# Optimization experiments

Measured on AMD Instinct MI355X. Metric: run time of the kernel, lower is better.

The kernel has to match this reference:

```python
import jax, jax.numpy as jnp
import numpy as np

B, C, H, W = 64, 8, 256, 256
EMB, LAT = 64, 32


def affine_grid(theta, Hh, Ww):
    # F.affine_grid, align_corners=False. theta: [N,2,3] -> grid [N,H,W,2] (x,y)
    xs = (jnp.arange(Ww, dtype=theta.dtype) + 0.5) * (2.0 / Ww) - 1.0
    ys = (jnp.arange(Hh, dtype=theta.dtype) + 0.5) * (2.0 / Hh) - 1.0
    X, Y = jnp.meshgrid(xs, ys)  # [H,W]
    base = jnp.stack([X, Y, jnp.ones_like(X)], axis=-1)  # [H,W,3]
    return jnp.einsum('hwk,nik->nhwi', base, theta)


def grid_sample(img, grid):
    # F.grid_sample bilinear, padding_mode='zeros', align_corners=False
    # img: [N,C,H,W], grid: [N,H,W,2]
    N, Cc, Hh, Ww = img.shape
    ix = ((grid[..., 0] + 1.0) * Ww - 1.0) * 0.5
    iy = ((grid[..., 1] + 1.0) * Hh - 1.0) * 0.5
    x0 = jnp.floor(ix)
    y0 = jnp.floor(iy)
    wx1 = ix - x0
    wy1 = iy - y0
    wx0 = 1.0 - wx1
    wy0 = 1.0 - wy1

    def gather(xf, yf):
        xi = xf.astype(jnp.int32)
        yi = yf.astype(jnp.int32)
        valid = ((xi >= 0) & (xi < Ww) & (yi >= 0) & (yi < Hh)).astype(img.dtype)
        xc = jnp.clip(xi, 0, Ww - 1)
        yc = jnp.clip(yi, 0, Hh - 1)

        def one(im, yb, xb, vb):
            return im[:, yb, xb] * vb[None]  # [C,H,W]

        return jax.vmap(one)(img, yc, xc, valid)

    v00 = gather(x0, y0)
    v01 = gather(x0 + 1.0, y0)
    v10 = gather(x0, y0 + 1.0)
    v11 = gather(x0 + 1.0, y0 + 1.0)
    w00 = (wy0 * wx0)[:, None]
    w01 = (wy0 * wx1)[:, None]
    w10 = (wy1 * wx0)[:, None]
    w11 = (wy1 * wx1)[:, None]
    return v00 * w00 + v01 * w01 + v10 * w10 + v11 * w11


def setup_inputs() -> dict:
    key = jax.random.key(0)
    ks = jax.random.split(key, 9)
    return {
        'x': jax.random.normal(ks[0], (B, C, H, W), jnp.float32),
        'W_ae': jax.random.normal(ks[1], (C, EMB), jnp.float32) * 0.1,
        'W_rot': jax.random.normal(ks[2], (EMB, 6), jnp.float32) * 0.1,
        'W_scale': jax.random.normal(ks[3], (EMB, 6), jnp.float32) * 0.1,
        'W_shear': jax.random.normal(ks[4], (EMB, 6), jnp.float32) * 0.1,
        'W_trans': jax.random.normal(ks[5], (EMB, 6), jnp.float32) * 0.1,
        'W_mask': jax.random.normal(ks[6], (EMB, 1), jnp.float32) * 0.1,
        'W_enc': jax.random.normal(ks[7], (C, LAT), jnp.float32) * 0.1,
        'W_dec': jax.random.normal(ks[8], (C, C), jnp.float32) * 0.1,
    }


def reference(x, W_ae, W_rot, W_scale, W_shear, W_trans, W_mask, W_enc, W_dec):
    Bb, Cc, Hh, Ww = x.shape
    # affine_encoder: global-average-pool + linear
    emb_affine = x.mean(axis=(2, 3)) @ W_ae  # [B,EMB]
    eye = jnp.array([[1.0, 0.0, 0.0], [0.0, 1.0, 0.0]], x.dtype)
    head = lambda Wt: (emb_affine @ Wt).reshape(Bb, 2, 3) * 0.1 + eye
    rotation = head(W_rot)
    scale = head(W_scale)
    shear = head(W_shear)
    translation = head(W_trans)
    mask_parameter = jax.nn.sigmoid(emb_affine @ W_mask)[:, :, None, None]  # [B,1,1,1]

    # affine_transform: four sequential affine_grid + grid_sample passes, then mask
    xt = x
    for theta in (rotation, scale, shear, translation):
        grid = affine_grid(theta, Hh, Ww)
        xt = grid_sample(xt, grid)
    xt = xt * mask_parameter

    emb = xt.mean(axis=(2, 3)) @ W_enc  # encoder on transformed image
    x_dec = jnp.einsum('bchw,cd->bdhw', xt, W_dec)  # pointwise-linear decoder
    return (x_dec, emb, scale, shear, rotation, translation, mask_parameter)
```

## Files before the change

### kernel.cpp

```cpp
#include <hip/hip_runtime.h>
#include <hip/hip_fp16.h>
#include <math.h>

#define BB   64
#define CC   8
#define HH   256
#define WW   256
#define EMB  64
#define LAT  32
#define HW   (HH*WW)
#define PLANE 65536
#define IMG  (CC*HW)

#define OFF_XDEC  0
#define OFF_EMB   33554432
#define OFF_SCALE 33556480
#define OFF_SHEAR 33556864
#define OFF_ROT   33557248
#define OFF_TRANS 33557632
#define OFF_MASK  33558016

#define WS_SUMS   0
#define WS_THETA  512
#define WS_MASK   2048
#define WS_ACC    2112
#define WS_BUF0   4096
#define WS_BUF1   (4096 + 16777216)

#define TH 16
#define TW 64
#define SR 20
#define SC 68
#define SN (SR*SC)

__global__ void k_zero(float* __restrict__ ws) {
    ws[WS_SUMS + threadIdx.x] = 0.f;
}

__device__ __forceinline__ unsigned pack2(float a, float b) {
    __half2 t = __floats2half2_rn(a, b);
    return *(unsigned*)&t;
}
__device__ __forceinline__ float2 up2(unsigned v) {
    __half2 h = *(__half2*)&v;
    return __half22float2(h);
}

__global__ void k_meanT(const float* __restrict__ x, uint4* __restrict__ outp,
                        float* __restrict__ sums) {
    int bid = blockIdx.x;
    int b = bid >> 6;
    int hq = bid & 63;
    int r = threadIdx.x >> 6;
    int lane = threadIdx.x & 63;
    int h = hq * 4 + r;
    const float* ib = x + (size_t)b * IMG + h * WW + 4 * lane;
    float4 v0 = *(const float4*)(ib + 0 * PLANE);
    float4 v1 = *(const float4*)(ib + 1 * PLANE);
    float4 v2 = *(const float4*)(ib + 2 * PLANE);
    float4 v3 = *(const float4*)(ib + 3 * PLANE);
    float4 v4 = *(const float4*)(ib + 4 * PLANE);
    float4 v5 = *(const float4*)(ib + 5 * PLANE);
    float4 v6 = *(const float4*)(ib + 6 * PLANE);
    float4 v7 = *(const float4*)(ib + 7 * PLANE);

    uint4* ob = outp + (size_t)b * HW + h * WW + 4 * lane;
#define PIXOUT(J, COMP) { uint4 u; \
    u.x = pack2(v0.COMP, v1.COMP); u.y = pack2(v2.COMP, v3.COMP); \
    u.z = pack2(v4.COMP, v5.COMP); u.w = pack2(v6.COMP, v7.COMP); ob[J] = u; }
    PIXOUT(0, x) PIXOUT(1, y) PIXOUT(2, z) PIXOUT(3, w)
#undef PIXOUT

    float p[CC];
    p[0] = (v0.x + v0.y) + (v0.z + v0.w);
    p[1] = (v1.x + v1.y) + (v1.z + v1.w);
    p[2] = (v2.x + v2.y) + (v2.z + v2.w);
    p[3] = (v3.x + v3.y) + (v3.z + v3.w);
    p[4] = (v4.x + v4.y) + (v4.z + v4.w);
    p[5] = (v5.x + v5.y) + (v5.z + v5.w);
    p[6] = (v6.x + v6.y) + (v6.z + v6.w);
    p[7] = (v7.x + v7.y) + (v7.z + v7.w);

    __shared__ float part[4][CC];
    #pragma unroll
    for (int ch = 0; ch < CC; ch++) {
        float v = p[ch];
        for (int off = 32; off > 0; off >>= 1) v += __shfl_down(v, off, 64);
        if (lane == 0) part[r][ch] = v;
    }
    __syncthreads();
    if (threadIdx.x < CC) {
        float v = (part[0][threadIdx.x] + part[1][threadIdx.x]) +
                  (part[2][threadIdx.x] + part[3][threadIdx.x]);
        atomicAdd(&sums[b * CC + threadIdx.x], v);
    }
}

__global__ void k_params(const float* __restrict__ sums,
                         const float* __restrict__ W_ae, const float* __restrict__ W_rot,
                         const float* __restrict__ W_scale, const float* __restrict__ W_shear,
                         const float* __restrict__ W_trans, const float* __restrict__ W_mask,
                         float* __restrict__ ws, float* __restrict__ out) {
    int b = blockIdx.x;
    int t = threadIdx.x;

    if (t < CC) ws[WS_ACC + b * CC + t] = 0.f;

    __shared__ float emb_s[EMB];
    {
        float s = 0.f;
        #pragma unroll
        for (int c = 0; c < CC; c++)
            s += (sums[b * CC + c] * (1.0f / (float)HW)) * W_ae[c * EMB + t];
        emb_s[t] = s;
    }
    __syncthreads();

    if (t < 24) {
        int h = t / 6, k = t % 6;
        const float* Wt = (h == 0) ? W_rot : (h == 1) ? W_scale : (h == 2) ? W_shear : W_trans;
        float s = 0.f;
        #pragma unroll
        for (int e = 0; e < EMB; e++) s += emb_s[e] * Wt[e * 6 + k];
        const float eyev = (k == 0 || k == 4) ? 1.0f : 0.0f;
        float th = s * 0.1f + eyev;
        ws[WS_THETA + h * (BB * 6) + b * 6 + k] = th;
        int off = (h == 0) ? OFF_ROT : (h == 1) ? OFF_SCALE : (h == 2) ? OFF_SHEAR : OFF_TRANS;
        out[off + b * 6 + k] = th;
    } else if (t == 24) {
        float s = 0.f;
        #pragma unroll
        for (int e = 0; e < EMB; e++) s += emb_s[e] * W_mask[e];
        float mk = 1.0f / (1.0f + expf(-s));
        ws[WS_MASK + b] = mk;
        out[OFF_MASK + b] = mk;
    }
}

struct Corners {
    int x0c, x1c, y0c, y1c;
    float w00, w01, w10, w11;
};

__device__ __forceinline__ Corners affine_corners(float t00, float t01, float t02,
                                                  float t10, float t11, float t12,
                                                  int gh, int gw) {
    float X = ((float)gw + 0.5f) * (2.0f / (float)WW) - 1.0f;
    float Y = ((float)gh + 0.5f) * (2.0f / (float)HH) - 1.0f;
    float gx = X * t00 + Y * t01 + t02;
    float gy = X * t10 + Y * t11 + t12;
    float ix = ((gx + 1.0f) * (float)WW - 1.0f) * 0.5f;
    float iy = ((gy + 1.0f) * (float)HH - 1.0f) * 0.5f;
    float x0f = floorf(ix), y0f = floorf(iy);
    int x0 = (int)x0f, y0 = (int)y0f, x1 = x0 + 1, y1 = y0 + 1;
    float wx1 = ix - x0f, wy1 = iy - y0f, wx0 = 1.f - wx1, wy0 = 1.f - wy1;
    float fx0 = ((unsigned)x0 < (unsigned)WW) ? 1.f : 0.f;
    float fx1 = ((unsigned)x1 < (unsigned)WW) ? 1.f : 0.f;
    float fy0 = ((unsigned)y0 < (unsigned)HH) ? 1.f : 0.f;
    float fy1 = ((unsigned)y1 < (unsigned)HH) ? 1.f : 0.f;
    Corners c;
    c.x0c = min(max(x0, 0), WW - 1); c.x1c = min(max(x1, 0), WW - 1);
    c.y0c = min(max(y0, 0), HH - 1); c.y1c = min(max(y1, 0), HH - 1);
    c.w00 = wy0*wx0*fy0*fx0; c.w01 = wy0*wx1*fy0*fx1;
    c.w10 = wy1*wx0*fy1*fx0; c.w11 = wy1*wx1*fy1*fx1;
    return c;
}

__device__ __forceinline__ uint4 bilerp8_pk(uint4 a00, uint4 a01, uint4 a10, uint4 a11,
                                            __half2 h00, __half2 h01, __half2 h10, __half2 h11) {
    uint4 u;
#define BLEND(COMP) { \
    __half2 r = __hmul2(*(__half2*)&a00.COMP, h00); \
    r = __hfma2(*(__half2*)&a01.COMP, h01, r); \
    r = __hfma2(*(__half2*)&a10.COMP, h10, r); \
    r = __hfma2(*(__half2*)&a11.COMP, h11, r); \
    u.COMP = *(unsigned*)&r; }
    BLEND(x) BLEND(y) BLEND(z) BLEND(w)
#undef BLEND
    return u;
}

__device__ __forceinline__ int lidx(int sr, int sc) {
    sr = min(max(sr, 0), SR - 1);
    sc = min(max(sc, 0), SC - 1);
    return sr * SC + (sc ^ ((sc >> 3) & 7));
}

__device__ __forceinline__ void stage_g2l(uint4* __restrict__ buf,
                                          const uint4* __restrict__ pb,
                                          const float* __restrict__ th,
                                          int oh, int ow, int tid) {
    float t00 = th[0], t01 = th[1], t02 = th[2], t10 = th[3], t11 = th[4], t12 = th[5];
    for (int i = tid; i < SN; i += 256) {
        int lr = i / SC, lc = i - lr * SC;
        Corners c = affine_corners(t00, t01, t02, t10, t11, t12, oh - 2 + lr, ow - 2 + lc);
        uint4 a00 = pb[c.y0c * WW + c.x0c], a01 = pb[c.y0c * WW + c.x1c];
        uint4 a10 = pb[c.y1c * WW + c.x0c], a11 = pb[c.y1c * WW + c.x1c];
        __half2 h00 = __float2half2_rn(c.w00), h01 = __float2half2_rn(c.w01);
        __half2 h10 = __float2half2_rn(c.w10), h11 = __float2half2_rn(c.w11);
        buf[lr * SC + (lc ^ ((lc >> 3) & 7))] =
            bilerp8_pk(a00, a01, a10, a11, h00, h01, h10, h11);
    }
}

__global__ __launch_bounds__(256) void k_warpA(const uint4* __restrict__ in,
                                               uint4* __restrict__ out,
                                               const float* __restrict__ ws) {
    __shared__ uint4 buf[SN];
    int bid = blockIdx.x;
    int b = bid >> 6;
    int tile = bid & 63;
    int oh = (tile >> 2) * TH;
    int ow = (tile & 3) * TW;
    int tid = threadIdx.x;
    const uint4* pb = in + (size_t)b * HW;

    stage_g2l(buf, pb, ws + WS_THETA + 0 * (BB * 6) + b * 6, oh, ow, tid);
    __syncthreads();

    const float* th = ws + WS_THETA + 1 * (BB * 6) + b * 6;
    float t00 = th[0], t01 = th[1], t02 = th[2], t10 = th[3], t11 = th[4], t12 = th[5];
    uint4* ob = out + (size_t)b * HW;
    for (int i = tid; i < TH * TW; i += 256) {
        int lr = i >> 6, lc = i & 63;
        int gh = oh + lr, gw = ow + lc;
        Corners c = affine_corners(t00, t01, t02, t10, t11, t12, gh, gw);
        uint4 a00 = buf[lidx(c.y0c - oh + 2, c.x0c - ow + 2)];
        uint4 a01 = buf[lidx(c.y0c - oh + 2, c.x1c - ow + 2)];
        uint4 a10 = buf[lidx(c.y1c - oh + 2, c.x0c - ow + 2)];
        uint4 a11 = buf[lidx(c.y1c - oh + 2, c.x1c - ow + 2)];
        __half2 h00 = __float2half2_rn(c.w00), h01 = __float2half2_rn(c.w01);
        __half2 h10 = __float2half2_rn(c.w10), h11 = __float2half2_rn(c.w11);
        ob[gh * WW + gw] = bilerp8_pk(a00, a01, a10, a11, h00, h01, h10, h11);
    }
}

__global__ __launch_bounds__(256) void k_warpB(const uint4* __restrict__ in,
                                               const float* __restrict__ ws,
                                               const float* __restrict__ W_dec,
                                               float* __restrict__ out,
                                               float* __restrict__ acc) {
    __shared__ uint4 buf[SN];
    __shared__ float Wd[CC * CC];
    __shared__ float part[4][CC];
    int bid = blockIdx.x;
    int b = bid >> 6;
    int tile = bid & 63;
    int oh = (tile >> 2) * TH;
    int ow = (tile & 3) * TW;
    int tid = threadIdx.x;
    if (tid < CC * CC) Wd[tid] = W_dec[tid];
    const uint4* pb = in + (size_t)b * HW;

    stage_g2l(buf, pb, ws + WS_THETA + 2 * (BB * 6) + b * 6, oh, ow, tid);
    __syncthreads();

    float mk = ws[WS_MASK + b];
    const float* th = ws + WS_THETA + 3 * (BB * 6) + b * 6;
    float t00 = th[0], t01 = th[1], t02 = th[2], t10 = th[3], t11 = th[4], t12 = th[5];

    int wv = tid >> 6, lane = tid & 63;
    int r = wv * 4 + (lane >> 4);
    int c0 = (lane & 15) * 4;
    float sl[CC];
    #pragma unroll
    for (int ch = 0; ch < CC; ch++) sl[ch] = 0.f;
    float od[CC][4];

    #pragma unroll
    for (int px = 0; px < 4; px++) {
        int gh = oh + r, gw = ow + c0 + px;
        Corners c = affine_corners(t00, t01, t02, t10, t11, t12, gh, gw);
        uint4 a00 = buf[lidx(c.y0c - oh + 2, c.x0c - ow + 2)];
        uint4 a01 = buf[lidx(c.y0c - oh + 2, c.x1c - ow + 2)];
        uint4 a10 = buf[lidx(c.y1c - oh + 2, c.x0c - ow + 2)];
        uint4 a11 = buf[lidx(c.y1c - oh + 2, c.x1c - ow + 2)];
        __half2 h00 = __float2half2_rn(c.w00 * mk), h01 = __float2half2_rn(c.w01 * mk);
        __half2 h10 = __float2half2_rn(c.w10 * mk), h11 = __float2half2_rn(c.w11 * mk);
        uint4 u = bilerp8_pk(a00, a01, a10, a11, h00, h01, h10, h11);

        float2 s01 = up2(u.x), s23 = up2(u.y), s45 = up2(u.z), s67 = up2(u.w);
        float s[CC] = {s01.x, s01.y, s23.x, s23.y, s45.x, s45.y, s67.x, s67.y};

        #pragma unroll
        for (int ch = 0; ch < CC; ch++) sl[ch] += s[ch];
        #pragma unroll
        for (int d = 0; d < CC; d++) {
            float rr = 0.f;
            #pragma unroll
            for (int ch = 0; ch < CC; ch++) rr += s[ch] * Wd[ch * CC + d];
            od[d][px] = rr;
        }
    }

    size_t base = (size_t)b * IMG + (size_t)(oh + r) * WW + (ow + c0);
    #pragma unroll
    for (int d = 0; d < CC; d++) {
        float4 f4 = make_float4(od[d][0], od[d][1], od[d][2], od[d][3]);
        *(float4*)(out + OFF_XDEC + base + d * PLANE) = f4;
    }

    #pragma unroll
    for (int ch = 0; ch < CC; ch++) {
        float v = sl[ch];
        for (int off = 32; off > 0; off >>= 1) v += __shfl_down(v, off, 64);
        if (lane == 0) part[wv][ch] = v;
    }
    __syncthreads();
    if (tid < CC) {
        float v = (part[0][tid] + part[1][tid]) + (part[2][tid] + part[3][tid]);
        atomicAdd(&acc[b * CC + tid], v);
    }
}

__global__ void k_emb(const float* __restrict__ acc, const float* __restrict__ W_enc,
                      float* __restrict__ out) {
    for (int i = threadIdx.x; i < BB * LAT; i += 256) {
        int b = i >> 5, l = i & 31;
        float s = 0.f;
        #pragma unroll
        for (int c = 0; c < CC; c++)
            s += (acc[b * CC + c] * (1.0f / (float)HW)) * W_enc[c * LAT + l];
        out[OFF_EMB + i] = s;
    }
}

extern "C" void kernel_launch(void* const* d_in, const int* in_sizes, int n_in,
                              void* d_out, int out_size, void* d_ws, size_t ws_size,
                              hipStream_t stream) {
    const float* x       = (const float*)d_in[0];
    const float* W_ae    = (const float*)d_in[1];
    const float* W_rot   = (const float*)d_in[2];
    const float* W_scale = (const float*)d_in[3];
    const float* W_shear = (const float*)d_in[4];
    const float* W_trans = (const float*)d_in[5];
    const float* W_mask  = (const float*)d_in[6];
    const float* W_enc   = (const float*)d_in[7];
    const float* W_dec   = (const float*)d_in[8];

    float* ws   = (float*)d_ws;
    float* out  = (float*)d_out;
    float* sums = ws + WS_SUMS;
    float* acc  = ws + WS_ACC;
    uint4* hb0  = (uint4*)(ws + WS_BUF0);
    uint4* hb1  = (uint4*)(ws + WS_BUF1);

    k_zero<<<1, 512, 0, stream>>>(ws);
    k_meanT<<<BB * (HH / 4), 256, 0, stream>>>(x, hb0, sums);
    k_params<<<BB, 64, 0, stream>>>(sums, W_ae, W_rot, W_scale, W_shear, W_trans, W_mask, ws, out);
    k_warpA<<<BB * 64, 256, 0, stream>>>(hb0, hb1, ws);
    k_warpB<<<BB * 64, 256, 0, stream>>>(hb1, ws, W_dec, out, acc);
    k_emb<<<1, 256, 0, stream>>>(acc, W_enc, out);
}
```

Before: 150.3 us.

## Double warp tile height to 32 rows with 512-thread blocks and packed-FMA decoder

Raises the output tile in both warp kernels from 16 to 32 rows and the block size to 512 threads, so the 2-row staging halo is a smaller share of each tile and less redundant first-pass resampling is done. In the second warp kernel the 8x8 decoder matmul now uses two-wide float vector FMAs with weights stored as pairs in shared memory, which may map to packed FMA instructions. Larger LDS per block (about 39KB) and half as many blocks may lower occupancy and leave fewer blocks per CU for load balancing.

```diff
diff --git a/kernel.cpp b/kernel.cpp
--- a/kernel.cpp
+++ b/kernel.cpp
@@ -27,11 +27,13 @@
 #define WS_BUF0   4096
 #define WS_BUF1   (4096 + 16777216)
 
-#define TH 16
+#define TH 32
 #define TW 64
-#define SR 20
+#define SR 36
 #define SC 68
 #define SN (SR*SC)
+
+typedef float v2f __attribute__((ext_vector_type(2)));
 
 __global__ void k_zero(float* __restrict__ ws) {
     ws[WS_SUMS + threadIdx.x] = 0.f;
@@ -186,12 +188,13 @@
     return sr * SC + (sc ^ ((sc >> 3) & 7));
 }
 
+template<int NT>
 __device__ __forceinline__ void stage_g2l(uint4* __restrict__ buf,
                                           const uint4* __restrict__ pb,
                                           const float* __restrict__ th,
                                           int oh, int ow, int tid) {
     float t00 = th[0], t01 = th[1], t02 = th[2], t10 = th[3], t11 = th[4], t12 = th[5];
-    for (int i = tid; i < SN; i += 256) {
+    for (int i = tid; i < SN; i += NT) {
         int lr = i / SC, lc = i - lr * SC;
         Corners c = affine_corners(t00, t01, t02, t10, t11, t12, oh - 2 + lr, ow - 2 + lc);
         uint4 a00 = pb[c.y0c * WW + c.x0c], a01 = pb[c.y0c * WW + c.x1c];
@@ -203,25 +206,25 @@
     }
 }
 
-__global__ __launch_bounds__(256) void k_warpA(const uint4* __restrict__ in,
+__global__ __launch_bounds__(512) void k_warpA(const uint4* __restrict__ in,
                                                uint4* __restrict__ out,
                                                const float* __restrict__ ws) {
     __shared__ uint4 buf[SN];
     int bid = blockIdx.x;
-    int b = bid >> 6;
-    int tile = bid & 63;
+    int b = bid >> 5;
+    int tile = bid & 31;
     int oh = (tile >> 2) * TH;
     int ow = (tile & 3) * TW;
     int tid = threadIdx.x;
     const uint4* pb = in + (size_t)b * HW;
 
-    stage_g2l(buf, pb, ws + WS_THETA + 0 * (BB * 6) + b * 6, oh, ow, tid);
+    stage_g2l<512>(buf, pb, ws + WS_THETA + 0 * (BB * 6) + b * 6, oh, ow, tid);
     __syncthreads();
 
     const float* th = ws + WS_THETA + 1 * (BB * 6) + b * 6;
     float t00 = th[0], t01 = th[1], t02 = th[2], t10 = th[3], t11 = th[4], t12 = th[5];
     uint4* ob = out + (size_t)b * HW;
-    for (int i = tid; i < TH * TW; i += 256) {
+    for (int i = tid; i < TH * TW; i += 512) {
         int lr = i >> 6, lc = i & 63;
         int gh = oh + lr, gw = ow + lc;
         Corners c = affine_corners(t00, t01, t02, t10, t11, t12, gh, gw);
@@ -235,24 +238,28 @@
     }
 }
 
-__global__ __launch_bounds__(256) void k_warpB(const uint4* __restrict__ in,
+__global__ __launch_bounds__(512) void k_warpB(const uint4* __restrict__ in,
                                                const float* __restrict__ ws,
                                                const float* __restrict__ W_dec,
                                                float* __restrict__ out,
                                                float* __restrict__ acc) {
     __shared__ uint4 buf[SN];
-    __shared__ float Wd[CC * CC];
-    __shared__ float part[4][CC];
+    __shared__ v2f Wd2[CC][4];
+    __shared__ float part[8][CC];
     int bid = blockIdx.x;
-    int b = bid >> 6;
-    int tile = bid & 63;
+    int b = bid >> 5;
+    int tile = bid & 31;
     int oh = (tile >> 2) * TH;
     int ow = (tile & 3) * TW;
     int tid = threadIdx.x;
-    if (tid < CC * CC) Wd[tid] = W_dec[tid];
+    if (tid < CC * 4) {
+        int ch = tid >> 2, j = tid & 3;
+        v2f w; w.x = W_dec[ch * CC + 2 * j]; w.y = W_dec[ch * CC + 2 * j + 1];
+        Wd2[ch][j] = w;
+    }
     const uint4* pb = in + (size_t)b * HW;
 
-    stage_g2l(buf, pb, ws + WS_THETA + 2 * (BB * 6) + b * 6, oh, ow, tid);
+    stage_g2l<512>(buf, pb, ws + WS_THETA + 2 * (BB * 6) + b * 6, oh, ow, tid);
     __syncthreads();
 
     float mk = ws[WS_MASK + b];
@@ -284,13 +291,19 @@
 
         #pragma unroll
         for (int ch = 0; ch < CC; ch++) sl[ch] += s[ch];
-        #pragma unroll
-        for (int d = 0; d < CC; d++) {
-            float rr = 0.f;
+
+        v2f o2[4];
+        #pragma unroll
+        for (int j = 0; j < 4; j++) { o2[j].x = 0.f; o2[j].y = 0.f; }
+        #pragma unroll
+        for (int ch = 0; ch < CC; ch++) {
+            v2f sb; sb.x = s[ch]; sb.y = s[ch];
             #pragma unroll
-            for (int ch = 0; ch < CC; ch++) rr += s[ch] * Wd[ch * CC + d];
-            od[d][px] = rr;
+            for (int j = 0; j < 4; j++)
+                o2[j] = __builtin_elementwise_fma(sb, Wd2[ch][j], o2[j]);
         }
+        #pragma unroll
+        for (int j = 0; j < 4; j++) { od[2*j][px] = o2[j].x; od[2*j+1][px] = o2[j].y; }
     }
 
     size_t base = (size_t)b * IMG + (size_t)(oh + r) * WW + (ow + c0);
@@ -308,7 +321,9 @@
     }
     __syncthreads();
     if (tid < CC) {
-        float v = (part[0][tid] + part[1][tid]) + (part[2][tid] + part[3][tid]);
+        float v = 0.f;
+        #pragma unroll
+        for (int w = 0; w < 8; w++) v += part[w][tid];
         atomicAdd(&acc[b * CC + tid], v);
     }
 }
@@ -348,7 +363,7 @@
     k_zero<<<1, 512, 0, stream>>>(ws);
     k_meanT<<<BB * (HH / 4), 256, 0, stream>>>(x, hb0, sums);
     k_params<<<BB, 64, 0, stream>>>(sums, W_ae, W_rot, W_scale, W_shear, W_trans, W_mask, ws, out);
-    k_warpA<<<BB * 64, 256, 0, stream>>>(hb0, hb1, ws);
-    k_warpB<<<BB * 64, 256, 0, stream>>>(hb1, ws, W_dec, out, acc);
+    k_warpA<<<BB * 32, 512, 0, stream>>>(hb0, hb1, ws);
+    k_warpB<<<BB * 32, 512, 0, stream>>>(hb1, ws, W_dec, out, acc);
     k_emb<<<1, 256, 0, stream>>>(acc, W_enc, out);
 }
```

Result: no change. 153.3 us (+2.0%).
